# Optimization experiments

Measured on AMD Instinct MI355X. Metric: run time of the kernel, lower is better.

## Reference

```python
import jax, jax.numpy as jnp
import numpy as np

N = 500_000      # total nodes in batched graph
B = 2_048        # number of graphs (segments)
D = 256          # input_dim == hidden_dim == output_dim


def setup_inputs() -> dict:
    key = jax.random.key(0)
    k = jax.random.split(key, 8)
    feat = jax.random.normal(k[0], (N, D), dtype=jnp.float32)
    cnt = jax.random.uniform(k[1], (N,), dtype=jnp.float32)
    segment_ids = jnp.sort(jax.random.randint(k[2], (N,), 0, B, dtype=jnp.int32))
    last_nodes = jax.random.randint(k[3], (B,), 0, N, dtype=jnp.int32)
    # learned parameters (torch nn.Linear: y = x @ W.T + b)
    s = 1.0 / np.sqrt(D)
    W_u = jax.random.uniform(k[4], (D, D), dtype=jnp.float32, minval=-s, maxval=s)
    W_v = jax.random.uniform(k[5], (D, D), dtype=jnp.float32, minval=-s, maxval=s)
    b_v = jax.random.uniform(k[6], (D,), dtype=jnp.float32, minval=-s, maxval=s)
    w_e = jax.random.uniform(k[7], (D,), dtype=jnp.float32, minval=-s, maxval=s)
    return {"feat": feat, "cnt": cnt, "segment_ids": segment_ids,
            "last_nodes": last_nodes, "W_u": W_u, "W_v": W_v,
            "b_v": b_v, "w_e": w_e}


def reference(feat, cnt, segment_ids, last_nodes, W_u, W_v, b_v, w_e):
    # fc_u: per-node projection  [N, D]
    feat_u = feat @ W_u.T
    # fc_v on last node of each graph, then broadcast back to nodes
    feat_v = feat[last_nodes] @ W_v.T + b_v          # [B, D]
    feat_vb = feat_v[segment_ids]                    # [N, D] broadcast_nodes
    # fc_e(sigmoid(u + v)) -> scalar gate per node
    e = jax.nn.sigmoid(feat_u + feat_vb) @ w_e       # [N]
    alpha = e * cnt                                  # [N]
    # segment-sum readout over graphs
    rst = jax.ops.segment_sum(feat * alpha[:, None], segment_ids,
                              num_segments=B)        # [B, D]
    return rst
```

## Files before the change

kernel.cpp:

```cpp
#include <hip/hip_runtime.h>
#include <hip/hip_bf16.h>

typedef __attribute__((ext_vector_type(8))) short short8;
typedef __attribute__((ext_vector_type(4))) float f32x4;

#define D 256
#define MT 64
#define NW 8
#define GRID_MAIN 256
#define GV 16

#define BAR_LGKM asm volatile("s_waitcnt lgkmcnt(0)\ns_barrier" ::: "memory")

__device__ __forceinline__ unsigned pack2(float a, float b) {
    __hip_bfloat162 hh = __float22bfloat162_rn(make_float2(a, b));
    return *(unsigned*)&hh;
}
__device__ __forceinline__ float fast_sigmoid(float x) {
    return __builtin_amdgcn_rcpf(1.f + __expf(-x));
}
__device__ __forceinline__ void dma16(const void* g, void* lds) {
    __builtin_amdgcn_global_load_lds((const __attribute__((address_space(1))) unsigned int*)g,
                                     (__attribute__((address_space(3))) unsigned int*)lds, 16, 0, 0);
}
__device__ __forceinline__ void dma4(const void* g, void* lds) {
    __builtin_amdgcn_global_load_lds((const __attribute__((address_space(1))) unsigned int*)g,
                                     (__attribute__((address_space(3))) unsigned int*)lds, 4, 0, 0);
}

__global__ __launch_bounds__(256) void k_prep(
    const float* __restrict__ feat, const int* __restrict__ last_nodes,
    const float* __restrict__ Wv, const float* __restrict__ bv,
    const float* __restrict__ Wu, unsigned short* __restrict__ Wub,
    float* __restrict__ featv, float* __restrict__ rst, int Bseg, int nOut) {
    const int b = blockIdx.x;
    const int t = threadIdx.x;
    if (b < 128) {
        __shared__ float fln[GV][D];
        const int b0 = b * GV;
        for (int g = 0; g < GV; ++g) {
            int bb = b0 + g;
            int ln = (bb < Bseg) ? last_nodes[bb] : 0;
            fln[g][t] = feat[(long)ln * D + t];
        }
        __syncthreads();
        float acc[GV];
        float bvj = bv[t];
        #pragma unroll
        for (int g = 0; g < GV; ++g) acc[g] = bvj;
        const float* wr = Wv + (long)t * D;
        for (int k = 0; k < D; k += 4) {
            float4 w4 = *(const float4*)(wr + k);
            #pragma unroll
            for (int g = 0; g < GV; ++g) {
                acc[g] += w4.x * fln[g][k]     + w4.y * fln[g][k + 1]
                        + w4.z * fln[g][k + 2] + w4.w * fln[g][k + 3];
            }
        }
        for (int g = 0; g < GV; ++g)
            if (b0 + g < Bseg) featv[(long)(b0 + g) * D + t] = acc[g];
    } else if (b < 384) {
        int i = (b - 128) * 256 + t;
        if (i < D * D) Wub[i] = (unsigned short)(pack2(Wu[i], 0.f) & 0xffffu);
    } else {
        int base = (b - 384) * 1024 + t;
        #pragma unroll
        for (int it = 0; it < 4; ++it) {
            int i = base + it * 256;
            if (i < nOut) rst[i] = 0.f;
        }
    }
}

__global__ __launch_bounds__(512, 2) void k_main(
    const float* __restrict__ feat, const float* __restrict__ cnt,
    const int* __restrict__ seg, const unsigned short* __restrict__ Wub,
    const float* __restrict__ featv, const float* __restrict__ we,
    float* __restrict__ rst, int N) {

    __shared__ float stageF[MT][D];
    __shared__ unsigned short Abuf[2][MT][D];
    __shared__ int   seg_s[4][MT];
    __shared__ float cnt_s[4][MT];
    __shared__ float e_s[NW][MT];
    __shared__ float alpha_s[MT];

    const int t  = threadIdx.x;
    const int w  = t >> 6;
    const int l  = t & 63;
    const int rl = l & 15;
    const int h  = l >> 4;

    const int T   = (N + MT - 1) / MT;
    const int nb  = gridDim.x;
    const int per = T / nb, rem = T % nb;
    const int bid = blockIdx.x;
    const int c0  = bid * per + (bid < rem ? bid : rem);
    const int c1  = c0 + per + (bid < rem ? 1 : 0);
    if (c0 >= c1) return;

#define STAGE(ti)                                                             \
    {                                                                         \
        const long nb0 = (long)(ti) * MT;                                     \
        long nsx = nb0 + l; if (nsx > (long)N - 1) nsx = (long)N - 1;         \
        dma4(seg + nsx, &seg_s[(ti) & 3][0]);                                 \
        dma4(cnt + nsx, &cnt_s[(ti) & 3][0]);                                 \
        asm volatile("" ::: "memory");                                        \
        _Pragma("unroll")                                                     \
        for (int i = 0; i < 8; ++i) {                                         \
            int r = w + 8 * i;                                                \
            long nn = nb0 + r; if (nn > (long)N - 1) nn = (long)N - 1;        \
            dma16(feat + nn * D + 4 * l, &stageF[r][0]);                      \
        }                                                                     \
    }

#define CONVERT(buf)                                                          \
    {                                                                         \
        _Pragma("unroll")                                                     \
        for (int i = 0; i < 8; ++i) {                                         \
            int r = w + 8 * i;                                                \
            f32x4 fv = *(const f32x4*)&stageF[r][4 * l];                      \
            *(uint2*)&Abuf[buf][r][(((l >> 1) ^ (r & 7)) << 3) + ((l & 1) << 2)] = \
                make_uint2(pack2(fv[0], fv[1]), pack2(fv[2], fv[3]));         \
        }                                                                     \
    }

    short8 a_reg[2][8];
    {
        const unsigned short* ab = Wub + (long)(32 * w + rl) * D + h * 8;
        #pragma unroll
        for (int mt = 0; mt < 2; ++mt)
            #pragma unroll
            for (int s = 0; s < 8; ++s)
                a_reg[mt][s] = *(const short8*)(ab + (long)mt * 16 * D + s * 32);
    }
    f32x4 wev[2];
    wev[0] = *(const f32x4*)(we + 32 * w + h * 4);
    wev[1] = *(const f32x4*)(we + 32 * w + 16 + h * 4);

    f32x4 fvr[2][4];
    STAGE(c0);
    asm volatile("s_waitcnt vmcnt(0)" ::: "memory");
    CONVERT(c0 & 1);
    {
        #pragma unroll
        for (int nt = 0; nt < 4; ++nt) {
            int sg = seg_s[c0 & 3][nt * 16 + rl];
            const float* fb = featv + (long)sg * D + 32 * w + h * 4;
            fvr[0][nt] = *(const f32x4*)(fb);
            fvr[1][nt] = *(const f32x4*)(fb + 16);
        }
    }
    asm volatile("" ::: "memory");
    if (c0 + 1 < c1) STAGE(c0 + 1);
    BAR_LGKM;

    for (int tt = c0; tt < c1; ++tt) {
        const long n0 = (long)tt * MT;
        const bool more1 = (tt + 1 < c1);
        const bool more2 = (tt + 2 < c1);
        const int  cur   = tt & 1;
        const int* seg_t = seg_s[tt & 3];

        f32x4 acc[2][4];
        #pragma unroll
        for (int mt = 0; mt < 2; ++mt)
            #pragma unroll
            for (int nt = 0; nt < 4; ++nt) acc[mt][nt] = (f32x4)0.f;

        const unsigned short* Ab = &Abuf[cur][0][0];
        #pragma unroll
        for (int s = 0; s < 8; ++s) {
            short8 bfr[4];
            #pragma unroll
            for (int nt = 0; nt < 4; ++nt) {
                int R  = nt * 16 + rl;
                int gr = (s * 4 + h) ^ (rl & 7);
                bfr[nt] = *(const short8*)(Ab + R * D + gr * 8);
            }
            #pragma unroll
            for (int mt = 0; mt < 2; ++mt)
                #pragma unroll
                for (int nt = 0; nt < 4; ++nt)
                    acc[mt][nt] = __builtin_amdgcn_mfma_f32_16x16x32_bf16(a_reg[mt][s], bfr[nt], acc[mt][nt], 0, 0, 0);
        }

        float ep[4] = {0.f, 0.f, 0.f, 0.f};
        #pragma unroll
        for (int mt = 0; mt < 2; ++mt)
            #pragma unroll
            for (int nt = 0; nt < 4; ++nt)
                #pragma unroll
                for (int r = 0; r < 4; ++r)
                    ep[nt] += wev[mt][r] * fast_sigmoid(acc[mt][nt][r] + fvr[mt][nt][r]);
        #pragma unroll
        for (int nt = 0; nt < 4; ++nt) {
            ep[nt] += __shfl_xor(ep[nt], 16);
            ep[nt] += __shfl_xor(ep[nt], 32);
        }
        if (h == 0) {
            #pragma unroll
            for (int nt = 0; nt < 4; ++nt) e_s[w][nt * 16 + rl] = ep[nt];
        }
        BAR_LGKM;

        if (t < MT) {
            float e = 0.f;
            #pragma unroll
            for (int q = 0; q < NW; ++q) e += e_s[q][t];
            alpha_s[t] = (n0 + t < N) ? e * cnt_s[tt & 3][t] : 0.f;
        }
        BAR_LGKM;

        long rb_p = -1; float ca_p = 0.f, cb_p = 0.f;
        {
            const int p   = t & 127;
            const int gq  = t >> 7;
            const int i0  = gq * 16;
            const int nv  = (int)(((long)N - n0 < MT) ? ((long)N - n0) : MT);
            const int i1  = (i0 + 16 < nv) ? (i0 + 16) : nv;
            const unsigned* Ab32 = (const unsigned*)Ab;
            if (i0 < i1) {
                if ((i1 - i0) == 16 && seg_t[i0] == seg_t[i1 - 1]) {
                    float ca = 0.f, cb = 0.f, ca2 = 0.f, cb2 = 0.f;
                    #pragma unroll
                    for (int i2 = 0; i2 < 16; i2 += 2) {
                        int i = i0 + i2;
                        unsigned v0 = Ab32[(i + 0) * 128 + (((p >> 2) ^ ((i + 0) & 7)) << 2) + (p & 3)];
                        unsigned v1 = Ab32[(i + 1) * 128 + (((p >> 2) ^ ((i + 1) & 7)) << 2) + (p & 3)];
                        float a0 = alpha_s[i + 0], a1 = alpha_s[i + 1];
                        ca  += __uint_as_float(v0 << 16) * a0;
                        cb  += __uint_as_float(v0 & 0xffff0000u) * a0;
                        ca2 += __uint_as_float(v1 << 16) * a1;
                        cb2 += __uint_as_float(v1 & 0xffff0000u) * a1;
                    }
                    rb_p = (long)seg_t[i0] * D + 2 * p;
                    ca_p = ca + ca2; cb_p = cb + cb2;
                } else {
                    float ca = 0.f, cb = 0.f;
                    int curseg = seg_t[i0];
                    for (int i = i0; i < i1; ++i) {
                        int sgi = seg_t[i];
                        if (sgi != curseg) {
                            long rb = (long)curseg * D + 2 * p;
                            atomicAdd(&rst[rb], ca); atomicAdd(&rst[rb + 1], cb);
                            ca = cb = 0.f; curseg = sgi;
                        }
                        unsigned v = Ab32[i * 128 + (((p >> 2) ^ (i & 7)) << 2) + (p & 3)];
                        float al = alpha_s[i];
                        ca += __uint_as_float(v << 16) * al;
                        cb += __uint_as_float(v & 0xffff0000u) * al;
                    }
                    rb_p = (long)curseg * D + 2 * p;
                    ca_p = ca; cb_p = cb;
                }
            }
        }
        asm volatile("" ::: "memory");

        if (more1) {
            asm volatile("s_waitcnt vmcnt(0)" ::: "memory");
            CONVERT((tt + 1) & 1);
        }

        if (more1) {
            const int* sn = seg_s[(tt + 1) & 3];
            #pragma unroll
            for (int nt = 0; nt < 4; ++nt) {
                int sg = sn[nt * 16 + rl];
                const float* fb = featv + (long)sg * D + 32 * w + h * 4;
                fvr[0][nt] = *(const f32x4*)(fb);
                fvr[1][nt] = *(const f32x4*)(fb + 16);
            }
            asm volatile("" ::: "memory");
        }

        if (rb_p >= 0) {
            atomicAdd(&rst[rb_p], ca_p);
            atomicAdd(&rst[rb_p + 1], cb_p);
        }
        asm volatile("" ::: "memory");

        if (more2) {
            STAGE(tt + 2);
            asm volatile("" ::: "memory");
        }

        BAR_LGKM;
    }
#undef STAGE
#undef CONVERT
}

extern "C" void kernel_launch(void* const* d_in, const int* in_sizes, int n_in,
                              void* d_out, int out_size, void* d_ws, size_t ws_size,
                              hipStream_t stream) {
    const float* feat = (const float*)d_in[0];
    const float* cnt  = (const float*)d_in[1];
    const int*   segp = (const int*)d_in[2];
    const int*   last = (const int*)d_in[3];
    const float* Wu   = (const float*)d_in[4];
    const float* Wv   = (const float*)d_in[5];
    const float* bv   = (const float*)d_in[6];
    const float* we   = (const float*)d_in[7];
    float* rst = (float*)d_out;

    const int N    = in_sizes[1];
    const int Bseg = in_sizes[3];

    unsigned short* Wub   = (unsigned short*)d_ws;
    float*          featv = (float*)((char*)d_ws + (size_t)D * D * sizeof(unsigned short));

    const int zero_blocks = (out_size + 1023) / 1024;
    k_prep<<<384 + zero_blocks, 256, 0, stream>>>(feat, last, Wv, bv, Wu, Wub, featv, rst, Bseg, out_size);
    k_main<<<GRID_MAIN, 512, 0, stream>>>(feat, cnt, segp, Wub, featv, we, rst, N);
}
```

Measured before the change: 190.2 us.

## Defer segment-sum readout by one tile and halve featv rows per prep block

The per-tile weighted segment-sum now runs for the previous tile, in the same barrier interval as the current tile's MFMA and sigmoid epilogue. alpha_s is double-buffered and the final tile is drained after the loop. This removes one block-wide barrier per tile and lets the LDS-bound readout overlap with the gate computation. In k_prep, GV drops from 16 to 8, so featv uses twice as many blocks for more parallelism. The cost is extra LDS for alpha and a tail step, and correctness depends on buffer indices not colliding across the prefetch ring.

```diff
diff --git a/kernel.cpp b/kernel.cpp
--- a/kernel.cpp
+++ b/kernel.cpp
@@ -8,7 +8,7 @@
 #define MT 64
 #define NW 8
 #define GRID_MAIN 256
-#define GV 16
+#define GV 8
 
 #define BAR_LGKM asm volatile("s_waitcnt lgkmcnt(0)\ns_barrier" ::: "memory")
 
@@ -26,6 +26,52 @@
 __device__ __forceinline__ void dma4(const void* g, void* lds) {
     __builtin_amdgcn_global_load_lds((const __attribute__((address_space(1))) unsigned int*)g,
                                      (__attribute__((address_space(3))) unsigned int*)lds, 4, 0, 0);
+}
+
+__device__ __forceinline__ void p4_run(
+    const unsigned* __restrict__ Ab32, const float* __restrict__ al_s,
+    const int* __restrict__ seg_t, long n0, int N, int t,
+    float* __restrict__ rst, long& rb_p, float& ca_p, float& cb_p) {
+    const int p   = t & 127;
+    const int gq  = t >> 7;
+    const int i0  = gq * 16;
+    const int nv  = (int)(((long)N - n0 < MT) ? ((long)N - n0) : MT);
+    const int i1  = (i0 + 16 < nv) ? (i0 + 16) : nv;
+    rb_p = -1; ca_p = 0.f; cb_p = 0.f;
+    if (i0 >= i1) return;
+    if ((i1 - i0) == 16 && seg_t[i0] == seg_t[i1 - 1]) {
+        float ca = 0.f, cb = 0.f, ca2 = 0.f, cb2 = 0.f;
+        #pragma unroll
+        for (int i2 = 0; i2 < 16; i2 += 2) {
+            int i = i0 + i2;
+            unsigned v0 = Ab32[(i + 0) * 128 + (((p >> 2) ^ ((i + 0) & 7)) << 2) + (p & 3)];
+            unsigned v1 = Ab32[(i + 1) * 128 + (((p >> 2) ^ ((i + 1) & 7)) << 2) + (p & 3)];
+            float a0 = al_s[i + 0], a1 = al_s[i + 1];
+            ca  += __uint_as_float(v0 << 16) * a0;
+            cb  += __uint_as_float(v0 & 0xffff0000u) * a0;
+            ca2 += __uint_as_float(v1 << 16) * a1;
+            cb2 += __uint_as_float(v1 & 0xffff0000u) * a1;
+        }
+        rb_p = (long)seg_t[i0] * D + 2 * p;
+        ca_p = ca + ca2; cb_p = cb + cb2;
+    } else {
+        float ca = 0.f, cb = 0.f;
+        int curseg = seg_t[i0];
+        for (int i = i0; i < i1; ++i) {
+            int sgi = seg_t[i];
+            if (sgi != curseg) {
+                long rb = (long)curseg * D + 2 * p;
+                atomicAdd(&rst[rb], ca); atomicAdd(&rst[rb + 1], cb);
+                ca = cb = 0.f; curseg = sgi;
+            }
+            unsigned v = Ab32[i * 128 + (((p >> 2) ^ (i & 7)) << 2) + (p & 3)];
+            float al = al_s[i];
+            ca += __uint_as_float(v << 16) * al;
+            cb += __uint_as_float(v & 0xffff0000u) * al;
+        }
+        rb_p = (long)curseg * D + 2 * p;
+        ca_p = ca; cb_p = cb;
+    }
 }
 
 __global__ __launch_bounds__(256) void k_prep(
@@ -35,7 +81,7 @@
     float* __restrict__ featv, float* __restrict__ rst, int Bseg, int nOut) {
     const int b = blockIdx.x;
     const int t = threadIdx.x;
-    if (b < 128) {
+    if (b < 256) {
         __shared__ float fln[GV][D];
         const int b0 = b * GV;
         for (int g = 0; g < GV; ++g) {
@@ -59,11 +105,11 @@
         }
         for (int g = 0; g < GV; ++g)
             if (b0 + g < Bseg) featv[(long)(b0 + g) * D + t] = acc[g];
-    } else if (b < 384) {
-        int i = (b - 128) * 256 + t;
+    } else if (b < 512) {
+        int i = (b - 256) * 256 + t;
         if (i < D * D) Wub[i] = (unsigned short)(pack2(Wu[i], 0.f) & 0xffffu);
     } else {
-        int base = (b - 384) * 1024 + t;
+        int base = (b - 512) * 1024 + t;
         #pragma unroll
         for (int it = 0; it < 4; ++it) {
             int i = base + it * 256;
@@ -83,7 +129,7 @@
     __shared__ int   seg_s[4][MT];
     __shared__ float cnt_s[4][MT];
     __shared__ float e_s[NW][MT];
-    __shared__ float alpha_s[MT];
+    __shared__ float alpha_s[2][MT];
 
     const int t  = threadIdx.x;
     const int w  = t >> 6;
@@ -160,7 +206,6 @@
         const bool more1 = (tt + 1 < c1);
         const bool more2 = (tt + 2 < c1);
         const int  cur   = tt & 1;
-        const int* seg_t = seg_s[tt & 3];
 
         f32x4 acc[2][4];
         #pragma unroll
@@ -202,61 +247,21 @@
             #pragma unroll
             for (int nt = 0; nt < 4; ++nt) e_s[w][nt * 16 + rl] = ep[nt];
         }
+
+        long rb_p = -1; float ca_p = 0.f, cb_p = 0.f;
+        if (tt > c0) {
+            p4_run((const unsigned*)&Abuf[(tt - 1) & 1][0][0],
+                   alpha_s[(tt - 1) & 1], seg_s[(tt - 1) & 3],
+                   (long)(tt - 1) * MT, N, t, rst, rb_p, ca_p, cb_p);
+        }
         BAR_LGKM;
 
         if (t < MT) {
             float e = 0.f;
             #pragma unroll
             for (int q = 0; q < NW; ++q) e += e_s[q][t];
-            alpha_s[t] = (n0 + t < N) ? e * cnt_s[tt & 3][t] : 0.f;
-        }
-        BAR_LGKM;
-
-        long rb_p = -1; float ca_p = 0.f, cb_p = 0.f;
-        {
-            const int p   = t & 127;
-            const int gq  = t >> 7;
-            const int i0  = gq * 16;
-            const int nv  = (int)(((long)N - n0 < MT) ? ((long)N - n0) : MT);
-            const int i1  = (i0 + 16 < nv) ? (i0 + 16) : nv;
-            const unsigned* Ab32 = (const unsigned*)Ab;
-            if (i0 < i1) {
-                if ((i1 - i0) == 16 && seg_t[i0] == seg_t[i1 - 1]) {
-                    float ca = 0.f, cb = 0.f, ca2 = 0.f, cb2 = 0.f;
-                    #pragma unroll
-                    for (int i2 = 0; i2 < 16; i2 += 2) {
-                        int i = i0 + i2;
-                        unsigned v0 = Ab32[(i + 0) * 128 + (((p >> 2) ^ ((i + 0) & 7)) << 2) + (p & 3)];
-                        unsigned v1 = Ab32[(i + 1) * 128 + (((p >> 2) ^ ((i + 1) & 7)) << 2) + (p & 3)];
-                        float a0 = alpha_s[i + 0], a1 = alpha_s[i + 1];
-                        ca  += __uint_as_float(v0 << 16) * a0;
-                        cb  += __uint_as_float(v0 & 0xffff0000u) * a0;
-                        ca2 += __uint_as_float(v1 << 16) * a1;
-                        cb2 += __uint_as_float(v1 & 0xffff0000u) * a1;
-                    }
-                    rb_p = (long)seg_t[i0] * D + 2 * p;
-                    ca_p = ca + ca2; cb_p = cb + cb2;
-                } else {
-                    float ca = 0.f, cb = 0.f;
-                    int curseg = seg_t[i0];
-                    for (int i = i0; i < i1; ++i) {
-                        int sgi = seg_t[i];
-                        if (sgi != curseg) {
-                            long rb = (long)curseg * D + 2 * p;
-                            atomicAdd(&rst[rb], ca); atomicAdd(&rst[rb + 1], cb);
-                            ca = cb = 0.f; curseg = sgi;
-                        }
-                        unsigned v = Ab32[i * 128 + (((p >> 2) ^ (i & 7)) << 2) + (p & 3)];
-                        float al = alpha_s[i];
-                        ca += __uint_as_float(v << 16) * al;
-                        cb += __uint_as_float(v & 0xffff0000u) * al;
-                    }
-                    rb_p = (long)curseg * D + 2 * p;
-                    ca_p = ca; cb_p = cb;
-                }
-            }
-        }
-        asm volatile("" ::: "memory");
+            alpha_s[cur][t] = (n0 + t < N) ? e * cnt_s[tt & 3][t] : 0.f;
+        }
 
         if (more1) {
             asm volatile("s_waitcnt vmcnt(0)" ::: "memory");
@@ -287,6 +292,18 @@
         }
 
         BAR_LGKM;
+    }
+
+    {
+        const int lt = c1 - 1;
+        long rb_p; float ca_p, cb_p;
+        p4_run((const unsigned*)&Abuf[lt & 1][0][0],
+               alpha_s[lt & 1], seg_s[lt & 3],
+               (long)lt * MT, N, t, rst, rb_p, ca_p, cb_p);
+        if (rb_p >= 0) {
+            atomicAdd(&rst[rb_p], ca_p);
+            atomicAdd(&rst[rb_p + 1], cb_p);
+        }
     }
 #undef STAGE
 #undef CONVERT
@@ -312,6 +329,6 @@
     float*          featv = (float*)((char*)d_ws + (size_t)D * D * sizeof(unsigned short));
 
     const int zero_blocks = (out_size + 1023) / 1024;
-    k_prep<<<384 + zero_blocks, 256, 0, stream>>>(feat, last, Wv, bv, Wu, Wub, featv, rst, Bseg, out_size);
+    k_prep<<<512 + zero_blocks, 256, 0, stream>>>(feat, last, Wv, bv, Wu, Wub, featv, rst, Bseg, out_size);
     k_main<<<GRID_MAIN, 512, 0, stream>>>(feat, cnt, segp, Wub, featv, we, rst, N);
 }
```

Result: faster. 178.7 us (-6.0%).
